# Performance work log

Measured on AMD Instinct MI355X. Metric: run time of the kernel, lower is better.

The kernel has to match this reference:

```python
import jax, jax.numpy as jnp
from jax import lax
import numpy as np

C = 256; NH = 8; NP = 4; FFN = 512; B = 2; H = 128; W = 128
HD = C // NH


def _ln(x, g, b):
    m = jnp.mean(x, -1, keepdims=True)
    v = jnp.var(x, -1, keepdims=True)
    return (x - m) * lax.rsqrt(v + 1e-5) * g + b


def _deform_attn(q, kv, off_w, off_b, attw_w, attw_b, vp_w, vp_b, op_w, op_b):
    # q, kv: (B, N, C) with N = H*W
    Bn, N, Cc = q.shape
    val = (kv @ vp_w + vp_b).reshape(Bn, N, NH, HD)
    off = (q @ off_w + off_b).reshape(Bn, N, NH, NP, 2)
    attw = jax.nn.softmax((q @ attw_w + attw_b).reshape(Bn, N, NH, NP), axis=-1)
    # identity-grid reference points (normalized, pixel centers)
    ry = (jnp.arange(H, dtype=q.dtype) + 0.5) / H
    rx = (jnp.arange(W, dtype=q.dtype) + 0.5) / W
    gy, gx = jnp.meshgrid(ry, rx, indexing='ij')
    ref = jnp.stack([gx.ravel(), gy.ravel()], -1)  # (N, 2) as (x, y)
    norm = jnp.array([W, H], dtype=q.dtype)
    loc = ref[None, :, None, None, :] + off / norm  # (B,N,NH,NP,2) in [0,1]
    # grid_sample align_corners=False, zeros padding
    x = loc[..., 0] * W - 0.5
    y = loc[..., 1] * H - 0.5
    x0 = jnp.floor(x); y0 = jnp.floor(y)
    lx = x - x0; ly = y - y0
    x0i = x0.astype(jnp.int32); y0i = y0.astype(jnp.int32)
    v_t = val.transpose(0, 2, 1, 3)  # (B, NH, N, HD)

    def gather(xi, yi, w):
        valid = (xi >= 0) & (xi < W) & (yi >= 0) & (yi < H)
        idx = jnp.clip(yi, 0, H - 1) * W + jnp.clip(xi, 0, W - 1)  # (B,N,NH,NP)
        idx_t = idx.transpose(0, 2, 1, 3).reshape(Bn, NH, N * NP)
        g = jnp.take_along_axis(v_t, idx_t[..., None], axis=2)
        g = g.reshape(Bn, NH, N, NP, HD)
        wm = (w * valid).transpose(0, 2, 1, 3)  # (B,NH,N,NP)
        return g * wm[..., None]

    samp = (gather(x0i, y0i, (1 - lx) * (1 - ly))
            + gather(x0i + 1, y0i, lx * (1 - ly))
            + gather(x0i, y0i + 1, (1 - lx) * ly)
            + gather(x0i + 1, y0i + 1, lx * ly))  # (B,NH,N,NP,HD)
    out = jnp.einsum('bhnpd,bnhp->bnhd', samp, attw).reshape(Bn, N, Cc)
    return out @ op_w + op_b


def _forward(cam_bev, sat_bev,
             c2s_off_w, c2s_off_b, c2s_attw_w, c2s_attw_b, c2s_vp_w, c2s_vp_b, c2s_op_w, c2s_op_b,
             s2c_off_w, s2c_off_b, s2c_attw_w, s2c_attw_b, s2c_vp_w, s2c_vp_b, s2c_op_w, s2c_op_b,
             ln1_g, ln1_b, ln2_g, ln2_b, lnf_g, lnf_b,
             ffn1_w, ffn1_b, ffn2_w, ffn2_b,
             g1_w, bn_g, bn_b, g2_w, g2_b):
    Bn, Cc, Hh, Ww = cam_bev.shape
    q_cam = cam_bev.reshape(Bn, Cc, Hh * Ww).transpose(0, 2, 1)
    q_sat = sat_bev.reshape(Bn, Cc, Hh * Ww).transpose(0, 2, 1)
    c2s = _deform_attn(q_cam, q_sat, c2s_off_w, c2s_off_b, c2s_attw_w, c2s_attw_b,
                       c2s_vp_w, c2s_vp_b, c2s_op_w, c2s_op_b)
    cam_att = _ln(q_cam + c2s, ln1_g, ln1_b)
    s2c = _deform_attn(q_sat, q_cam, s2c_off_w, s2c_off_b, s2c_attw_w, s2c_attw_b,
                       s2c_vp_w, s2c_vp_b, s2c_op_w, s2c_op_b)
    sat_att = _ln(q_sat + s2c, ln2_g, ln2_b)
    cam_map = cam_att.transpose(0, 2, 1).reshape(Bn, Cc, Hh, Ww)
    sat_map = sat_att.transpose(0, 2, 1).reshape(Bn, Cc, Hh, Ww)
    gi = jnp.concatenate([cam_map, sat_map], axis=1)
    h = lax.conv_general_dilated(gi, g1_w, (1, 1), 'SAME',
                                 dimension_numbers=('NCHW', 'OIHW', 'NCHW'))
    # BatchNorm2d in eval mode: running_mean=0, running_var=1
    h = jax.nn.relu(h * lax.rsqrt(jnp.float32(1.0 + 1e-5)) * bn_g[None, :, None, None]
                    + bn_b[None, :, None, None])
    g = jax.nn.sigmoid(jnp.einsum('bchw,oc->bohw', h, g2_w) + g2_b[None, :, None, None])
    fused = g * cam_map + (1 - g) * sat_map
    ff = fused.reshape(Bn, Cc, Hh * Ww).transpose(0, 2, 1)
    ff = ff + (jax.nn.relu(ff @ ffn1_w + ffn1_b) @ ffn2_w + ffn2_b)
    ff = _ln(ff, lnf_g, lnf_b)
    return ff.transpose(0, 2, 1).reshape(Bn, Cc, Hh, Ww) + cam_bev


def setup_inputs() -> dict:
    key = jax.random.key(0)
    ks = iter(jax.random.split(key, 40))

    def rn(shape, s=0.02):
        return jax.random.normal(next(ks), shape, jnp.float32) * s

    # directional offset-bias init (as in original init_weights)
    thetas = np.arange(NH) * (2.0 * np.pi / NH)
    grid = np.stack([np.cos(thetas), np.sin(thetas)], -1)
    grid = grid / np.abs(grid).max(-1, keepdims=True)
    grid = np.tile(grid[:, None, :], (1, NP, 1)) * np.arange(1, NP + 1)[None, :, None]
    off_bias = jnp.asarray(grid.reshape(-1), jnp.float32)

    def attn_params():
        return dict(off_w=rn((C, NH * NP * 2), 0.01), off_b=off_bias,
                    attw_w=rn((C, NH * NP), 0.02), attw_b=rn((NH * NP,), 0.02),
                    vp_w=rn((C, C), 0.05), vp_b=jnp.zeros((C,), jnp.float32),
                    op_w=rn((C, C), 0.05), op_b=jnp.zeros((C,), jnp.float32))

    p1 = attn_params(); p2 = attn_params()
    inp = {
        'cam_bev': jax.random.normal(next(ks), (B, C, H, W), jnp.float32),
        'sat_bev': jax.random.normal(next(ks), (B, C, H, W), jnp.float32),
    }
    for pre, p in (('c2s_', p1), ('s2c_', p2)):
        for k, v in p.items():
            inp[pre + k] = v
    inp.update(
        ln1_g=jnp.ones((C,), jnp.float32), ln1_b=jnp.zeros((C,), jnp.float32),
        ln2_g=jnp.ones((C,), jnp.float32), ln2_b=jnp.zeros((C,), jnp.float32),
        lnf_g=jnp.ones((C,), jnp.float32), lnf_b=jnp.zeros((C,), jnp.float32),
        ffn1_w=rn((C, FFN), 0.05), ffn1_b=jnp.zeros((FFN,), jnp.float32),
        ffn2_w=rn((FFN, C), 0.05), ffn2_b=jnp.zeros((C,), jnp.float32),
        g1_w=rn((C // 2, 2 * C, 3, 3), 0.02),
        bn_g=jnp.ones((C // 2,), jnp.float32), bn_b=jnp.zeros((C // 2,), jnp.float32),
        g2_w=rn((C, C // 2), 0.02), g2_b=jnp.zeros((C,), jnp.float32),
    )
    return inp


def reference(cam_bev, sat_bev,
              c2s_off_w, c2s_off_b, c2s_attw_w, c2s_attw_b, c2s_vp_w, c2s_vp_b, c2s_op_w, c2s_op_b,
              s2c_off_w, s2c_off_b, s2c_attw_w, s2c_attw_b, s2c_vp_w, s2c_vp_b, s2c_op_w, s2c_op_b,
              ln1_g, ln1_b, ln2_g, ln2_b, lnf_g, lnf_b,
              ffn1_w, ffn1_b, ffn2_w, ffn2_b,
              g1_w, bn_g, bn_b, g2_w, g2_b):
    return _forward(cam_bev, sat_bev,
                    c2s_off_w, c2s_off_b, c2s_attw_w, c2s_attw_b, c2s_vp_w, c2s_vp_b, c2s_op_w, c2s_op_b,
                    s2c_off_w, s2c_off_b, s2c_attw_w, s2c_attw_b, s2c_vp_w, s2c_vp_b, s2c_op_w, s2c_op_b,
                    ln1_g, ln1_b, ln2_g, ln2_b, lnf_g, lnf_b,
                    ffn1_w, ffn1_b, ffn2_w, ffn2_b,
                    g1_w, bn_g, bn_b, g2_w, g2_b)
```

## Files before the change

kernel.cpp:

```cpp
#include <hip/hip_runtime.h>
#include <hip/hip_bf16.h>
#include <cstddef>

#define BBn  2
#define CCn  256
#define HHn  128
#define WWn  128
#define NNn  (HHn*WWn)
#define MTOT (BBn*NNn)
#define PADW 130

typedef unsigned short u16;
typedef __attribute__((ext_vector_type(8))) short bf8v;
typedef __attribute__((ext_vector_type(8))) unsigned short u16x8;
typedef __attribute__((ext_vector_type(4))) float f4v;

typedef __attribute__((address_space(1))) const void gvoid_t;
typedef __attribute__((address_space(3))) void svoid_t;
#define ASYNC16(g, l) __builtin_amdgcn_global_load_lds((gvoid_t*)(g), (svoid_t*)(l), 16, 0, 0)

__device__ __forceinline__ u16 f2bf(float f) {
    __hip_bfloat16 h = __float2bfloat16(f);
    return *reinterpret_cast<u16*>(&h);
}
__device__ __forceinline__ float bf2f(u16 h) {
    return __uint_as_float(((unsigned)h) << 16);
}

struct ZOff {
    long a, w, bia, f1, f2, b1, r, p;
    int ch;
};

template<int BM, int BN, int WC, int EPI, int KK>
__global__ __launch_bounds__(256)
void mgemm(const u16* __restrict__ A, const u16* __restrict__ Wt,
           const float* __restrict__ bias, int ldw, int Nc,
           float* __restrict__ outf, float* __restrict__ outf2,
           u16* __restrict__ outb, const u16* __restrict__ img,
           const void* __restrict__ resid,
           const float* __restrict__ p0, const float* __restrict__ p1,
           int choff, ZOff zo)
{
    constexpr int WR = 4 / WC;
    constexpr int MROWS = BM / WR;
    constexpr int MI = MROWS / 16;
    constexpr int AT = BM / 64;
    constexpr int BT = BN / 64;
    constexpr int NSTEPS = KK / 32;

    __shared__ __align__(16) u16 As[2 * BM * 32];
    __shared__ __align__(16) u16 Bs[2 * BN * 32];
    __shared__ float red[4][64][2];

    const int z = blockIdx.z;
    if (z) {
        A += (long)z * zo.a; Wt += (long)z * zo.w;
        if (bias)  bias  += (long)z * zo.bia;
        if (outf)  outf  += (long)z * zo.f1;
        if (outf2) outf2 += (long)z * zo.f2;
        if (outb)  outb  += (long)z * zo.b1;
        if (p0)    p0    += (long)z * zo.p;
        if (p1)    p1    += (long)z * zo.p;
        choff += z * zo.ch;
    }

    const int tid  = threadIdx.x;
    const int lane = tid & 63;
    const int w    = tid >> 6;
    const int wr   = w / WC, wc = w % WC;
    const int by = blockIdx.y;
    const int m0 = by * BM;
    const int n0 = blockIdx.x * BN;
    const int lr = lane & 15, lq = lane >> 4;

    const u16* gA[AT]; int loA[AT];
    #pragma unroll
    for (int t = 0; t < AT; ++t) {
        int c = t * 256 + tid; int row = c >> 2; int part = c & 3;
        int pg = part ^ ((row >> 1) & 3);
        gA[t] = A + (size_t)(m0 + row) * KK + pg * 8;
        loA[t] = c * 8;
    }
    const u16* gB[BT]; int loB[BT];
    #pragma unroll
    for (int t = 0; t < BT; ++t) {
        int c = t * 256 + tid; int row = c >> 2; int part = c & 3;
        int pg = part ^ ((row >> 1) & 3);
        gB[t] = Wt + (size_t)(n0 + row) * ldw + pg * 8;
        loB[t] = c * 8;
    }

    f4v acc[MI][4];
    if constexpr (EPI == 7 || EPI == 9) {
        const u16* r16 = (const u16*)resid + (EPI == 7 ? (long)z * zo.r : 0);
        #pragma unroll
        for (int j = 0; j < 4; ++j) {
            int n = wc * 64 + j * 16 + lr;
            float bj = bias[n];
            #pragma unroll
            for (int i = 0; i < MI; ++i)
                #pragma unroll
                for (int r = 0; r < 4; ++r) {
                    int m = m0 + i * 16 + lq * 4 + r;
                    acc[i][j][r] = bf2f(r16[(size_t)m * 256 + n]) + bj;
                }
        }
    } else {
        #pragma unroll
        for (int i = 0; i < MI; ++i)
            #pragma unroll
            for (int j = 0; j < 4; ++j)
                acc[i][j] = (f4v){0.f, 0.f, 0.f, 0.f};
    }

    auto stageG = [&](int s, int buf) {
        int k0 = s * 32;
        #pragma unroll
        for (int t = 0; t < AT; ++t)
            ASYNC16(gA[t] + k0, (u16*)As + buf * (BM * 32) + loA[t]);
        #pragma unroll
        for (int t = 0; t < BT; ++t)
            ASYNC16(gB[t] + k0, (u16*)Bs + buf * (BN * 32) + loB[t]);
    };
    auto computeStep = [&](int s) {
        const u16* Ab = As + (s & 1) * (BM * 32);
        const u16* Bb = Bs + (s & 1) * (BN * 32);
        bf8v af[MI], bv[4];
        #pragma unroll
        for (int i = 0; i < MI; ++i) {
            int row = wr * MROWS + i * 16 + lr;
            af[i] = *(const bf8v*)&Ab[row * 32 + ((lq ^ ((row >> 1) & 3)) << 3)];
        }
        #pragma unroll
        for (int j = 0; j < 4; ++j) {
            int row = wc * 64 + j * 16 + lr;
            bv[j] = *(const bf8v*)&Bb[row * 32 + ((lq ^ ((row >> 1) & 3)) << 3)];
        }
        #pragma unroll
        for (int i = 0; i < MI; ++i)
            #pragma unroll
            for (int j = 0; j < 4; ++j)
                acc[i][j] = __builtin_amdgcn_mfma_f32_16x16x32_bf16(af[i], bv[j], acc[i][j], 0, 0, 0);
    };

    stageG(0, 0);
    __syncthreads();
    for (int s = 0; s < NSTEPS - 1; ++s) {
        stageG(s + 1, (s + 1) & 1);
        computeStep(s);
        __syncthreads();
    }
    computeStep(NSTEPS - 1);

    if constexpr (EPI == 7 || EPI == 9) {
        float g4[4], b4[4];
        #pragma unroll
        for (int j = 0; j < 4; ++j) {
            int n = wc * 64 + j * 16 + lr;
            g4[j] = p0[n]; b4[j] = p1[n];
        }
        #pragma unroll
        for (int i = 0; i < MI; ++i)
            #pragma unroll
            for (int r = 0; r < 4; ++r) {
                float p = 0.f, p2 = 0.f;
                #pragma unroll
                for (int j = 0; j < 4; ++j) { float v = acc[i][j][r]; p += v; p2 += v * v; }
                p += __shfl_xor(p, 1, 16);  p2 += __shfl_xor(p2, 1, 16);
                p += __shfl_xor(p, 2, 16);  p2 += __shfl_xor(p2, 2, 16);
                p += __shfl_xor(p, 4, 16);  p2 += __shfl_xor(p2, 4, 16);
                p += __shfl_xor(p, 8, 16);  p2 += __shfl_xor(p2, 8, 16);
                if (lr == 0) {
                    int row = i * 16 + lq * 4 + r;
                    red[w][row][0] = p; red[w][row][1] = p2;
                }
            }
        __syncthreads();
        #pragma unroll
        for (int i = 0; i < MI; ++i) {
            float mean4[4], rstd4[4];
            #pragma unroll
            for (int r = 0; r < 4; ++r) {
                int row = i * 16 + lq * 4 + r;
                float s  = red[0][row][0] + red[1][row][0] + red[2][row][0] + red[3][row][0];
                float s2 = red[0][row][1] + red[1][row][1] + red[2][row][1] + red[3][row][1];
                float mean = s * (1.f / 256.f);
                float var  = s2 * (1.f / 256.f) - mean * mean;
                mean4[r] = mean;
                rstd4[r] = rsqrtf(var + 1e-5f);
            }
            if constexpr (EPI == 7) {
                #pragma unroll
                for (int r = 0; r < 4; ++r) {
                    int m = m0 + i * 16 + lq * 4 + r;
                    int b = m >> 14, sp = m & (NNn - 1);
                    size_t pb = (((size_t)b * PADW + (sp >> 7) + 1) * PADW + (sp & 127) + 1) * 512 + choff;
                    #pragma unroll
                    for (int j = 0; j < 4; ++j) {
                        int n = wc * 64 + j * 16 + lr;
                        outb[pb + n] = f2bf((acc[i][j][r] - mean4[r]) * rstd4[r] * g4[j] + b4[j]);
                    }
                }
            } else {
                int mb = m0 + i * 16 + lq * 4;
                int b = mb >> 14, sp = mb & (NNn - 1);
                #pragma unroll
                for (int j = 0; j < 4; ++j) {
                    int n = wc * 64 + j * 16 + lr;
                    size_t oi = ((size_t)b * 256 + n) * NNn + sp;
                    float4 cv = *(const float4*)&outf2[oi];
                    float4 o;
                    o.x = (acc[i][j][0] - mean4[0]) * rstd4[0] * g4[j] + b4[j] + cv.x;
                    o.y = (acc[i][j][1] - mean4[1]) * rstd4[1] * g4[j] + b4[j] + cv.y;
                    o.z = (acc[i][j][2] - mean4[2]) * rstd4[2] * g4[j] + b4[j] + cv.z;
                    o.w = (acc[i][j][3] - mean4[3]) * rstd4[3] * g4[j] + b4[j] + cv.w;
                    *(float4*)&outf[oi] = o;
                }
            }
        }
        return;
    }

    float bj[4]; int ncol[4];
    #pragma unroll
    for (int j = 0; j < 4; ++j) {
        int n = n0 + wc * 64 + j * 16 + lr;
        ncol[j] = n;
        if constexpr (EPI == 0 || EPI == 4 || EPI == 5) bj[j] = bias[n];
    }
    #pragma unroll
    for (int i = 0; i < MI; ++i) {
        #pragma unroll
        for (int r = 0; r < 4; ++r) {
            int m = m0 + wr * MROWS + i * 16 + lq * 4 + r;
            size_t pb = 0;
            if constexpr (EPI == 4) {
                int b = m >> 14, sp = m & (NNn - 1);
                pb = (((size_t)b * PADW + (sp >> 7) + 1) * PADW + (sp & 127) + 1) * 512;
            }
            #pragma unroll
            for (int j = 0; j < 4; ++j) {
                int n = ncol[j];
                float v = acc[i][j][r];
                size_t oi = (size_t)m * Nc + n;
                if constexpr (EPI == 0) {
                    outb[oi] = f2bf(v + bj[j]);
                } else if constexpr (EPI == 2) {
                    if (n < 64)      outf [(size_t)m * 64 + n]        = v + p0[n];
                    else if (n < 96) outf2[(size_t)m * 32 + (n - 64)] = v + p1[n - 64];
                } else if constexpr (EPI == 4) {
                    float vv = v + bj[j];
                    float g = 1.f / (1.f + __expf(-vv));
                    float f = g * bf2f(img[pb + n]) + (1.f - g) * bf2f(img[pb + 256 + n]);
                    outb[oi] = f2bf(f);
                } else if constexpr (EPI == 5) {
                    outb[oi] = f2bf(fmaxf(v + bj[j], 0.f));
                }
            }
        }
    }
}

template<int TAPS>
__global__ __launch_bounds__(256)
void conv_k(const u16* __restrict__ img, const u16* __restrict__ Wt,
            float* __restrict__ outp)
{
    constexpr int NS = TAPS * 16;
    __shared__ __align__(16) u16 As[2 * 128 * 32];
    __shared__ __align__(16) u16 Bs[2 * 128 * 32];

    const int z = blockIdx.z;
    outp += (size_t)z * MTOT * 128;
    const int tid = threadIdx.x;
    const int lane = tid & 63;
    const int w = tid >> 6;
    const int wr = w >> 1, wc = w & 1;
    int by = blockIdx.y;
    by = ((by & 7) << 5) | (by >> 3);
    const int m0 = by * 128;
    const int lr = lane & 15, lq = lane >> 4;

    const u16* abase[2]; const u16* bbase[2]; int ldsOff[2];
    #pragma unroll
    for (int t = 0; t < 2; ++t) {
        int c = t * 256 + tid;
        int row = c >> 2, part = c & 3;
        int pg = part ^ ((row >> 1) & 3);
        ldsOff[t] = c * 8;
        int m = m0 + row; int b = m >> 14; int sp = m & (NNn - 1);
        long cb = ((long)b * PADW + (sp >> 7)) * PADW + (sp & 127);
        abase[t] = img + cb * 512 + pg * 8;
        bbase[t] = Wt + (size_t)row * 4608 + pg * 8;
    }

    long adel[TAPS]; int bdel[TAPS];
    #pragma unroll
    for (int tt = 0; tt < TAPS; ++tt) {
        int tap = z * TAPS + tt;
        int dy = tap / 3, dx = tap - dy * 3;
        adel[tt] = (long)(dy * PADW + dx) * 512;
        bdel[tt] = tap * 512;
    }

    f4v acc[4][4];
    #pragma unroll
    for (int i = 0; i < 4; ++i)
        #pragma unroll
        for (int j = 0; j < 4; ++j)
            acc[i][j] = (f4v){0.f, 0.f, 0.f, 0.f};

    auto stage = [&](int s, int buf) {
        int tt = s >> 4;
        int ci = (s & 15) * 32;
        #pragma unroll
        for (int t = 0; t < 2; ++t) {
            ASYNC16(abase[t] + adel[tt] + ci, (u16*)As + buf * (128 * 32) + ldsOff[t]);
            ASYNC16(bbase[t] + bdel[tt] + ci, (u16*)Bs + buf * (128 * 32) + ldsOff[t]);
        }
    };
    auto computeStep = [&](int s) {
        const u16* Ab = As + (s & 1) * (128 * 32);
        const u16* Bb = Bs + (s & 1) * (128 * 32);
        bf8v af[4], bv[4];
        #pragma unroll
        for (int i = 0; i < 4; ++i) {
            int row = wr * 64 + i * 16 + lr;
            af[i] = *(const bf8v*)&Ab[row * 32 + ((lq ^ ((row >> 1) & 3)) << 3)];
        }
        #pragma unroll
        for (int j = 0; j < 4; ++j) {
            int row = wc * 64 + j * 16 + lr;
            bv[j] = *(const bf8v*)&Bb[row * 32 + ((lq ^ ((row >> 1) & 3)) << 3)];
        }
        #pragma unroll
        for (int i = 0; i < 4; ++i)
            #pragma unroll
            for (int j = 0; j < 4; ++j)
                acc[i][j] = __builtin_amdgcn_mfma_f32_16x16x32_bf16(af[i], bv[j], acc[i][j], 0, 0, 0);
    };

    stage(0, 0);
    __syncthreads();
    #pragma unroll
    for (int s = 0; s < NS - 1; ++s) {
        stage(s + 1, (s + 1) & 1);
        computeStep(s);
        __syncthreads();
    }
    computeStep(NS - 1);

    #pragma unroll
    for (int i = 0; i < 4; ++i)
        #pragma unroll
        for (int r = 0; r < 4; ++r) {
            int m = m0 + wr * 64 + i * 16 + lq * 4 + r;
            #pragma unroll
            for (int j = 0; j < 4; ++j) {
                int n = wc * 64 + j * 16 + lr;
                outp[(size_t)m * 128 + n] = acc[i][j][r];
            }
        }
}

__global__ __launch_bounds__(256)
void combine_k(const float* __restrict__ part, const float* __restrict__ bng,
               const float* __restrict__ bnb, u16* __restrict__ hb)
{
    const float bnscale = rsqrtf(1.0f + 1e-5f);
    int i = (blockIdx.x * 256 + threadIdx.x) * 4;
    int n = i & 127;
    float4 a = *(const float4*)&part[i];
    float4 b = *(const float4*)&part[(size_t)MTOT * 128 + i];
    float4 c = *(const float4*)&part[(size_t)MTOT * 256 + i];
    ushort4 o;
    o.x = f2bf(fmaxf((a.x + b.x + c.x) * bnscale * bng[n + 0] + bnb[n + 0], 0.f));
    o.y = f2bf(fmaxf((a.y + b.y + c.y) * bnscale * bng[n + 1] + bnb[n + 1], 0.f));
    o.z = f2bf(fmaxf((a.z + b.z + c.z) * bnscale * bng[n + 2] + bnb[n + 2], 0.f));
    o.w = f2bf(fmaxf((a.w + b.w + c.w) * bnscale * bng[n + 3] + bnb[n + 3], 0.f));
    *(ushort4*)&hb[i] = o;
}

__global__ __launch_bounds__(256)
void tcvt_k(const float* __restrict__ cam, const float* __restrict__ sat,
            u16* __restrict__ qcam, u16* __restrict__ qsat)
{
    __shared__ float t[64][65];
    int z = blockIdx.z;
    const float* src = (z < 2) ? cam : sat;
    u16* dst = (z < 2) ? qcam : qsat;
    int b = z & 1;
    int c0 = blockIdx.x * 64, sp0 = blockIdx.y * 64;
    #pragma unroll
    for (int it = 0; it < 16; ++it) {
        int idx = it * 256 + threadIdx.x;
        int cl = idx >> 6, sl = idx & 63;
        t[cl][sl] = src[((size_t)(b * CCn + c0 + cl)) * NNn + sp0 + sl];
    }
    __syncthreads();
    #pragma unroll
    for (int it = 0; it < 16; ++it) {
        int idx = it * 256 + threadIdx.x;
        int sl = idx >> 6, cl = idx & 63;
        dst[((size_t)(b * NNn + sp0 + sl)) * CCn + c0 + cl] = f2bf(t[cl][sl]);
    }
}

__global__ __launch_bounds__(256)
void sample_k(const u16* __restrict__ val, const float* __restrict__ off,
              const float* __restrict__ lg, u16* __restrict__ outp)
{
    __shared__ uint2 desc[32][17];

    int z = blockIdx.z;
    val  += (size_t)z * MTOT * CCn;
    off  += (size_t)z * MTOT * 64;
    lg   += (size_t)z * MTOT * 32;
    outp += (size_t)z * MTOT * CCn;

    const int tid = threadIdx.x;
    const int rh0 = blockIdx.x * 32;

    if (tid < 32) {
        int rhg = rh0 + tid;
        int h = rhg & 7, rn = rhg >> 3;
        int n = rn & (NNn - 1), b = rn >> 14;
        int yp = n >> 7, xp = n & 127;

        const float* ofp = off + (size_t)rn * 64 + h * 8;
        const float* lgp = lg  + (size_t)rn * 32 + h * 4;
        float4 of0 = *(const float4*)ofp;
        float4 of1 = *(const float4*)(ofp + 4);
        float4 lgv = *(const float4*)lgp;
        float ofx[4] = { of0.x, of0.z, of1.x, of1.z };
        float ofy[4] = { of0.y, of0.w, of1.y, of1.w };

        float mx = fmaxf(fmaxf(lgv.x, lgv.y), fmaxf(lgv.z, lgv.w));
        float e0 = __expf(lgv.x - mx), e1 = __expf(lgv.y - mx);
        float e2 = __expf(lgv.z - mx), e3 = __expf(lgv.w - mx);
        float inv = 1.f / (e0 + e1 + e2 + e3);
        float aw[4] = { e0 * inv, e1 * inv, e2 * inv, e3 * inv };

        unsigned hb = (unsigned)(b * NNn) * 256u + h * 32;
        #pragma unroll
        for (int p = 0; p < 4; ++p) {
            float xs = (float)xp + ofx[p];
            float ys = (float)yp + ofy[p];
            float x0f = floorf(xs), y0f = floorf(ys);
            float lx = xs - x0f, ly = ys - y0f;
            int x0 = (int)x0f, y0 = (int)y0f;
            #pragma unroll
            for (int c = 0; c < 4; ++c) {
                int xi = x0 + (c & 1), yi = y0 + (c >> 1);
                bool valid = (xi >= 0) & (xi < WWn) & (yi >= 0) & (yi < HHn);
                float wgt = valid
                    ? aw[p] * ((c & 1) ? lx : 1.f - lx) * ((c >> 1) ? ly : 1.f - ly)
                    : 0.f;
                int xc = min(max(xi, 0), WWn - 1);
                int yc = min(max(yi, 0), HHn - 1);
                unsigned addr = hb + (unsigned)(yc * WWn + xc) * 256u;
                desc[tid][p * 4 + c] = make_uint2(addr, __float_as_uint(wgt));
            }
        }
    }
    __syncthreads();

    const int rh = tid >> 3;
    const int q  = tid & 7;
    const int rhg = rh0 + rh;
    const int h = rhg & 7, rn = rhg >> 3;

    float a0 = 0.f, a1 = 0.f, a2 = 0.f, a3 = 0.f;
    #pragma unroll
    for (int k = 0; k < 16; ++k) {
        uint2 d = desc[rh][k];
        float wgt = __uint_as_float(d.y);
        ushort4 v = *(const ushort4*)(val + d.x + q * 4);
        a0 += wgt * bf2f(v.x);
        a1 += wgt * bf2f(v.y);
        a2 += wgt * bf2f(v.z);
        a3 += wgt * bf2f(v.w);
    }
    ushort4 o;
    o.x = f2bf(a0); o.y = f2bf(a1); o.z = f2bf(a2); o.w = f2bf(a3);
    *(ushort4*)(outp + (size_t)rn * CCn + h * 32 + q * 4) = o;
}

__global__ __launch_bounds__(256)
void repack_all(const float* __restrict__ vp1, const float* __restrict__ op1,
                const float* __restrict__ vp2, const float* __restrict__ op2,
                const float* __restrict__ f1w, const float* __restrict__ f2w,
                const float* __restrict__ of1, const float* __restrict__ aw1,
                const float* __restrict__ of2, const float* __restrict__ aw2,
                const float* __restrict__ g1,  const float* __restrict__ g2,
                const float* __restrict__ vpb1, const float* __restrict__ vpb2,
                const float* __restrict__ opb1, const float* __restrict__ opb2,
                const float* __restrict__ ofb1, const float* __restrict__ awb1,
                const float* __restrict__ ofb2, const float* __restrict__ awb2,
                const float* __restrict__ l1g, const float* __restrict__ l1b,
                const float* __restrict__ l2g, const float* __restrict__ l2b,
                u16* __restrict__ wb, float* __restrict__ bb)
{
    int i = blockIdx.x * 256 + threadIdx.x;
    if (i >= 1212416 + 2240) return;
    if (i >= 1212416) {
        int j = i - 1212416;
        float v;
        if      (j < 256)  v = vpb1[j];
        else if (j < 512)  v = vpb2[j - 256];
        else if (j < 768)  v = opb1[j - 512];
        else if (j < 1024) v = opb2[j - 768];
        else if (j < 1088) v = ofb1[j - 1024];
        else if (j < 1120) v = awb1[j - 1088];
        else if (j < 1184) v = ofb2[j - 1120];
        else if (j < 1216) v = awb2[j - 1184];
        else if (j < 1472) v = l1g[j - 1216];
        else if (j < 1728) v = l1b[j - 1472];
        else if (j < 1984) v = l2g[j - 1728];
        else               v = l2b[j - 1984];
        bb[j] = v;
        return;
    }
    float v;
    if (i < 262144) {
        const float* src[4] = { vp1, vp2, op1, op2 };
        int q = i >> 16, j = i & 65535;
        int n = j >> 8, k = j & 255;
        v = src[q][(size_t)k * 256 + n];
    } else if (i < 393216) {
        int j = i - 262144; int n = j >> 8, k = j & 255;
        v = f1w[(size_t)k * 512 + n];
    } else if (i < 524288) {
        int j = i - 393216; int n = j >> 9, k = j & 511;
        v = f2w[(size_t)k * 256 + n];
    } else if (i < 589824) {
        int jj = i - 524288; int hh = jj >> 15; int j = jj & 32767;
        int n = j >> 8, k = j & 255;
        const float* ofw = hh ? of2 : of1;
        const float* aww = hh ? aw2 : aw1;
        if (n < 64)      v = ofw[(size_t)k * 64 + n];
        else if (n < 96) v = aww[(size_t)k * 32 + (n - 64)];
        else             v = 0.f;
    } else if (i < 1179648) {
        int j = i - 589824; int co = j / 4608, k = j - co * 4608;
        int tap = k >> 9, ci = k & 511;
        v = g1[((size_t)co * 512 + ci) * 9 + tap];
    } else {
        int j = i - 1179648; int n = j >> 7, k = j & 127;
        v = g2[(size_t)n * 128 + k];
    }
    wb[i] = f2bf(v);
}

extern "C" void kernel_launch(void* const* d_in, const int* in_sizes, int n_in,
                              void* d_out, int out_size, void* d_ws, size_t ws_size,
                              hipStream_t stream)
{
    const float* cam_bev   = (const float*)d_in[0];
    const float* sat_bev   = (const float*)d_in[1];
    const float* c2s_off_w  = (const float*)d_in[2];
    const float* c2s_off_b  = (const float*)d_in[3];
    const float* c2s_attw_w = (const float*)d_in[4];
    const float* c2s_attw_b = (const float*)d_in[5];
    const float* c2s_vp_w   = (const float*)d_in[6];
    const float* c2s_vp_b   = (const float*)d_in[7];
    const float* c2s_op_w   = (const float*)d_in[8];
    const float* c2s_op_b   = (const float*)d_in[9];
    const float* s2c_off_w  = (const float*)d_in[10];
    const float* s2c_off_b  = (const float*)d_in[11];
    const float* s2c_attw_w = (const float*)d_in[12];
    const float* s2c_attw_b = (const float*)d_in[13];
    const float* s2c_vp_w   = (const float*)d_in[14];
    const float* s2c_vp_b   = (const float*)d_in[15];
    const float* s2c_op_w   = (const float*)d_in[16];
    const float* s2c_op_b   = (const float*)d_in[17];
    const float* ln1_g = (const float*)d_in[18];
    const float* ln1_b = (const float*)d_in[19];
    const float* ln2_g = (const float*)d_in[20];
    const float* ln2_b = (const float*)d_in[21];
    const float* lnf_g = (const float*)d_in[22];
    const float* lnf_b = (const float*)d_in[23];
    const float* ffn1_w = (const float*)d_in[24];
    const float* ffn1_b = (const float*)d_in[25];
    const float* ffn2_w = (const float*)d_in[26];
    const float* ffn2_b = (const float*)d_in[27];
    const float* g1_w  = (const float*)d_in[28];
    const float* bn_g  = (const float*)d_in[29];
    const float* bn_b  = (const float*)d_in[30];
    const float* g2_w  = (const float*)d_in[31];
    const float* g2_b  = (const float*)d_in[32];

    char* base = (char*)d_ws;
    size_t off = 0;
    auto alloc = [&](size_t bytes) -> void* {
        void* p = base + off;
        off += (bytes + 255) & ~(size_t)255;
        return p;
    };

    u16*   qcam   = (u16*)  alloc((size_t)MTOT * CCn * 2 * 2);
    u16*   qsat   = qcam + (size_t)MTOT * CCn;
    u16*   valb   = (u16*)  alloc((size_t)MTOT * CCn * 2 * 2);
    u16*   sampb  = (u16*)  alloc((size_t)MTOT * CCn * 2 * 2);
    float* offb   = (float*)alloc((size_t)MTOT * 64 * 4 * 2);
    float* attwb  = (float*)alloc((size_t)MTOT * 32 * 4 * 2);
    size_t padBytes = (size_t)BBn * PADW * PADW * 512 * 2;
    u16*   pad    = (u16*)  alloc(padBytes);
    u16*   hbuf   = (u16*)  alloc((size_t)MTOT * 128 * 2);
    u16*   wbase  = (u16*)  alloc((size_t)1212416 * 2);
    float* biasbf = (float*)alloc((size_t)2240 * 4);
    u16* wvp = wbase;
    u16* wop = wbase + 131072;
    u16* wf1 = wbase + 262144;
    u16* wf2 = wbase + 393216;
    u16* woa = wbase + 524288;
    u16* wcv = wbase + 589824;
    u16* wg2 = wbase + 1179648;
    u16*   fused_bf = valb;
    float* convpart = (float*)sampb;
    u16*   midb     = qcam;

    dim3 blk(256);
    ZOff zz{0, 0, 0, 0, 0, 0, 0, 0, 0};

    hipMemsetAsync(pad, 0, padBytes, stream);
    tcvt_k<<<dim3(4, 256, 4), blk, 0, stream>>>(cam_bev, sat_bev, qcam, qsat);
    repack_all<<<4746, blk, 0, stream>>>(c2s_vp_w, c2s_op_w, s2c_vp_w, s2c_op_w,
                                         ffn1_w, ffn2_w, c2s_off_w, c2s_attw_w,
                                         s2c_off_w, s2c_attw_w, g1_w, g2_w,
                                         c2s_vp_b, s2c_vp_b, c2s_op_b, s2c_op_b,
                                         c2s_off_b, c2s_attw_b, s2c_off_b, s2c_attw_b,
                                         ln1_g, ln1_b, ln2_g, ln2_b,
                                         wbase, biasbf);

    {
        ZOff zo{ -(long)MTOT * CCn, 65536, 256, 0, 0, (long)MTOT * CCn, 0, 0, 0 };
        mgemm<128, 128, 2, 0, 256><<<dim3(2, 256, 2), blk, 0, stream>>>(
            qsat, wvp, biasbf, 256, 256,
            nullptr, nullptr, valb, nullptr, nullptr, nullptr, nullptr, 0, zo);
    }
    {
        ZOff zo{ (long)MTOT * CCn, 32768, 0, (long)MTOT * 64, (long)MTOT * 32, 0, 0, 96, 0 };
        mgemm<128, 128, 2, 2, 256><<<dim3(1, 256, 2), blk, 0, stream>>>(
            qcam, woa, nullptr, 256, 128,
            offb, attwb, nullptr, nullptr, nullptr, biasbf + 1024, biasbf + 1088, 0, zo);
    }
    sample_k<<<dim3(8192, 1, 2), blk, 0, stream>>>(valb, offb, attwb, sampb);
    {
        ZOff zo{ (long)MTOT * CCn, 65536, 256, 0, 0, 0, (long)MTOT * CCn, 512, 256 };
        mgemm<64, 256, 4, 7, 256><<<dim3(1, 512, 2), blk, 0, stream>>>(
            sampb, wop, biasbf + 512, 256, 256,
            nullptr, nullptr, pad, nullptr, qcam, biasbf + 1216, biasbf + 1472, 0, zo);
    }
    conv_k<3><<<dim3(1, 256, 3), blk, 0, stream>>>(pad, wcv, convpart);
    combine_k<<<4096, blk, 0, stream>>>(convpart, bn_g, bn_b, hbuf);

    mgemm<128, 128, 2, 4, 128><<<dim3(2, 256, 1), blk, 0, stream>>>(
        hbuf, wg2, g2_b, 128, 256,
        nullptr, nullptr, fused_bf, pad, nullptr, nullptr, nullptr, 0, zz);

    mgemm<128, 128, 2, 5, 256><<<dim3(4, 256, 1), blk, 0, stream>>>(
        fused_bf, wf1, ffn1_b, 256, 512,
        nullptr, nullptr, midb, nullptr, nullptr, nullptr, nullptr, 0, zz);
    mgemm<64, 256, 4, 9, 512><<<dim3(1, 512, 1), blk, 0, stream>>>(
        midb, wf2, ffn2_b, 512, 256,
        (float*)d_out, (float*)cam_bev, nullptr, nullptr, fused_bf, lnf_g, lnf_b, 0, zz);
}
```

Baseline: 298.7 us.

## Deepen conv GEMM prefetch to two stages and zero only padding ring

The conv GEMM main loop now issues loads two stages ahead. It uses explicit vmcnt waits and raw s_barrier instead of __syncthreads, so global-to-LDS transfers overlap more with MFMA work. Separately, the full hipMemset of the padded buffer is replaced by a small kernel that zeroes only the border ring, assuming the interior is overwritten later. Both rely on hand-tuned waitcnt counts and buffer-index reuse, which risks a race if the counts or the stage/buffer mapping are wrong.

```diff
diff --git a/kernel.cpp b/kernel.cpp
--- a/kernel.cpp
+++ b/kernel.cpp
@@ -342,14 +342,24 @@
     };
 
     stage(0, 0);
-    __syncthreads();
-    #pragma unroll
-    for (int s = 0; s < NS - 1; ++s) {
-        stage(s + 1, (s + 1) & 1);
+    stage(1, 1);
+    asm volatile("s_waitcnt vmcnt(4)" ::: "memory");
+    __builtin_amdgcn_s_barrier();
+    #pragma unroll 4
+    for (int s = 0; s < NS; ++s) {
         computeStep(s);
-        __syncthreads();
-    }
-    computeStep(NS - 1);
+        asm volatile("s_waitcnt lgkmcnt(0)" ::: "memory");
+        __builtin_amdgcn_sched_barrier(0);
+        __builtin_amdgcn_s_barrier();
+        if (s + 2 < NS) {
+            stage(s + 2, s & 1);
+            __builtin_amdgcn_sched_barrier(0);
+            asm volatile("s_waitcnt vmcnt(4)" ::: "memory");
+        } else {
+            asm volatile("s_waitcnt vmcnt(0)" ::: "memory");
+        }
+        __builtin_amdgcn_s_barrier();
+    }
 
     #pragma unroll
     for (int i = 0; i < 4; ++i)
@@ -380,6 +390,22 @@
     o.z = f2bf(fmaxf((a.z + b.z + c.z) * bnscale * bng[n + 2] + bnb[n + 2], 0.f));
     o.w = f2bf(fmaxf((a.w + b.w + c.w) * bnscale * bng[n + 3] + bnb[n + 3], 0.f));
     *(ushort4*)&hb[i] = o;
+}
+
+__global__ __launch_bounds__(256)
+void zring_k(u16* __restrict__ pad)
+{
+    int i = blockIdx.x * 256 + threadIdx.x;
+    if (i >= 66048) return;
+    int e = i * 8;
+    const int per_b = 264192;
+    int b = e / per_b; int r = e - b * per_b;
+    long off;
+    if (r < 66560)       { int x = r >> 9, c = r & 511;                 off = (((long)b * PADW + 0)   * PADW + x)   * 512 + c; }
+    else if (r < 133120) { int r2 = r - 66560;  int x = r2 >> 9, c = r2 & 511; off = (((long)b * PADW + 129) * PADW + x)   * 512 + c; }
+    else if (r < 198656) { int r2 = r - 133120; int y = (r2 >> 9) + 1, c = r2 & 511; off = (((long)b * PADW + y)   * PADW + 0)   * 512 + c; }
+    else                 { int r2 = r - 198656; int y = (r2 >> 9) + 1, c = r2 & 511; off = (((long)b * PADW + y)   * PADW + 129) * 512 + c; }
+    *(u16x8*)(pad + off) = (u16x8){0, 0, 0, 0, 0, 0, 0, 0};
 }
 
 __global__ __launch_bounds__(256)
@@ -624,7 +650,7 @@
     dim3 blk(256);
     ZOff zz{0, 0, 0, 0, 0, 0, 0, 0, 0};
 
-    hipMemsetAsync(pad, 0, padBytes, stream);
+    zring_k<<<258, blk, 0, stream>>>(pad);
     tcvt_k<<<dim3(4, 256, 4), blk, 0, stream>>>(cam_bev, sat_bev, qcam, qsat);
     repack_all<<<4746, blk, 0, stream>>>(c2s_vp_w, c2s_op_w, s2c_vp_w, s2c_op_w,
                                          ffn1_w, ffn2_w, c2s_off_w, c2s_attw_w,
```

Measured after the change: 296.6 us. Within noise of the previous version (-0.7%).

## Split conv into 9 bf16 tap partials, zero only pad ring, swizzle sample blocks

Applied to the files above, without the earlier changes.

The 3x3 conv is split-K over 9 single-tap slices instead of 3 three-tap slices, which triples the number of blocks. Partial sums are stored as bf16 and reduced over 9 slices in the combine kernel. The full memset of the padded buffer is replaced by a kernel that zeroes only the border ring, and sample_k block indices are swizzled for locality. The costs are extra partial traffic, bf16 rounding of the partials, and a separate 9x partial buffer.

```diff
diff --git a/kernel.cpp b/kernel.cpp
--- a/kernel.cpp
+++ b/kernel.cpp
@@ -265,7 +265,7 @@
 template<int TAPS>
 __global__ __launch_bounds__(256)
 void conv_k(const u16* __restrict__ img, const u16* __restrict__ Wt,
-            float* __restrict__ outp)
+            u16* __restrict__ outp)
 {
     constexpr int NS = TAPS * 16;
     __shared__ __align__(16) u16 As[2 * 128 * 32];
@@ -343,7 +343,7 @@
 
     stage(0, 0);
     __syncthreads();
-    #pragma unroll
+    #pragma unroll 4
     for (int s = 0; s < NS - 1; ++s) {
         stage(s + 1, (s + 1) & 1);
         computeStep(s);
@@ -359,27 +359,46 @@
             #pragma unroll
             for (int j = 0; j < 4; ++j) {
                 int n = wc * 64 + j * 16 + lr;
-                outp[(size_t)m * 128 + n] = acc[i][j][r];
+                outp[(size_t)m * 128 + n] = f2bf(acc[i][j][r]);
             }
         }
 }
 
 __global__ __launch_bounds__(256)
-void combine_k(const float* __restrict__ part, const float* __restrict__ bng,
+void combine_k(const u16* __restrict__ part, const float* __restrict__ bng,
                const float* __restrict__ bnb, u16* __restrict__ hb)
 {
     const float bnscale = rsqrtf(1.0f + 1e-5f);
     int i = (blockIdx.x * 256 + threadIdx.x) * 4;
     int n = i & 127;
-    float4 a = *(const float4*)&part[i];
-    float4 b = *(const float4*)&part[(size_t)MTOT * 128 + i];
-    float4 c = *(const float4*)&part[(size_t)MTOT * 256 + i];
+    float s0 = 0.f, s1 = 0.f, s2 = 0.f, s3 = 0.f;
+    #pragma unroll
+    for (int p = 0; p < 9; ++p) {
+        ushort4 a = *(const ushort4*)&part[(size_t)p * MTOT * 128 + i];
+        s0 += bf2f(a.x); s1 += bf2f(a.y); s2 += bf2f(a.z); s3 += bf2f(a.w);
+    }
     ushort4 o;
-    o.x = f2bf(fmaxf((a.x + b.x + c.x) * bnscale * bng[n + 0] + bnb[n + 0], 0.f));
-    o.y = f2bf(fmaxf((a.y + b.y + c.y) * bnscale * bng[n + 1] + bnb[n + 1], 0.f));
-    o.z = f2bf(fmaxf((a.z + b.z + c.z) * bnscale * bng[n + 2] + bnb[n + 2], 0.f));
-    o.w = f2bf(fmaxf((a.w + b.w + c.w) * bnscale * bng[n + 3] + bnb[n + 3], 0.f));
+    o.x = f2bf(fmaxf(s0 * bnscale * bng[n + 0] + bnb[n + 0], 0.f));
+    o.y = f2bf(fmaxf(s1 * bnscale * bng[n + 1] + bnb[n + 1], 0.f));
+    o.z = f2bf(fmaxf(s2 * bnscale * bng[n + 2] + bnb[n + 2], 0.f));
+    o.w = f2bf(fmaxf(s3 * bnscale * bng[n + 3] + bnb[n + 3], 0.f));
     *(ushort4*)&hb[i] = o;
+}
+
+__global__ __launch_bounds__(256)
+void zring_k(u16* __restrict__ pad)
+{
+    int i = blockIdx.x * 256 + threadIdx.x;
+    if (i >= 66048) return;
+    int e = i * 8;
+    const int per_b = 264192;
+    int b = e / per_b; int r = e - b * per_b;
+    long off;
+    if (r < 66560)       { int x = r >> 9, c = r & 511;                 off = (((long)b * PADW + 0)   * PADW + x)   * 512 + c; }
+    else if (r < 133120) { int r2 = r - 66560;  int x = r2 >> 9, c = r2 & 511; off = (((long)b * PADW + 129) * PADW + x)   * 512 + c; }
+    else if (r < 198656) { int r2 = r - 133120; int y = (r2 >> 9) + 1, c = r2 & 511; off = (((long)b * PADW + y)   * PADW + 0)   * 512 + c; }
+    else                 { int r2 = r - 198656; int y = (r2 >> 9) + 1, c = r2 & 511; off = (((long)b * PADW + y)   * PADW + 129) * 512 + c; }
+    *(u16x8*)(pad + off) = (u16x8){0, 0, 0, 0, 0, 0, 0, 0};
 }
 
 __global__ __launch_bounds__(256)
@@ -420,7 +439,9 @@
     outp += (size_t)z * MTOT * CCn;
 
     const int tid = threadIdx.x;
-    const int rh0 = blockIdx.x * 32;
+    int bx = blockIdx.x;
+    bx = ((bx & 7) << 10) | (bx >> 3);
+    const int rh0 = bx * 32;
 
     if (tid < 32) {
         int rhg = rh0 + tid;
@@ -608,6 +629,7 @@
     size_t padBytes = (size_t)BBn * PADW * PADW * 512 * 2;
     u16*   pad    = (u16*)  alloc(padBytes);
     u16*   hbuf   = (u16*)  alloc((size_t)MTOT * 128 * 2);
+    u16*   convpart = (u16*)alloc((size_t)9 * MTOT * 128 * 2);
     u16*   wbase  = (u16*)  alloc((size_t)1212416 * 2);
     float* biasbf = (float*)alloc((size_t)2240 * 4);
     u16* wvp = wbase;
@@ -618,13 +640,12 @@
     u16* wcv = wbase + 589824;
     u16* wg2 = wbase + 1179648;
     u16*   fused_bf = valb;
-    float* convpart = (float*)sampb;
     u16*   midb     = qcam;
 
     dim3 blk(256);
     ZOff zz{0, 0, 0, 0, 0, 0, 0, 0, 0};
 
-    hipMemsetAsync(pad, 0, padBytes, stream);
+    zring_k<<<258, blk, 0, stream>>>(pad);
     tcvt_k<<<dim3(4, 256, 4), blk, 0, stream>>>(cam_bev, sat_bev, qcam, qsat);
     repack_all<<<4746, blk, 0, stream>>>(c2s_vp_w, c2s_op_w, s2c_vp_w, s2c_op_w,
                                          ffn1_w, ffn2_w, c2s_off_w, c2s_attw_w,
@@ -653,7 +674,7 @@
             sampb, wop, biasbf + 512, 256, 256,
             nullptr, nullptr, pad, nullptr, qcam, biasbf + 1216, biasbf + 1472, 0, zo);
     }
-    conv_k<3><<<dim3(1, 256, 3), blk, 0, stream>>>(pad, wcv, convpart);
+    conv_k<1><<<dim3(1, 256, 9), blk, 0, stream>>>(pad, wcv, convpart);
     combine_k<<<4096, blk, 0, stream>>>(convpart, bn_g, bn_b, hbuf);
 
     mgemm<128, 128, 2, 4, 128><<<dim3(2, 256, 1), blk, 0, stream>>>(
```

New measurement: 306.8 us. 2.7% more time.
